# Kernel optimization log

Hardware: AMD Instinct MI355X
Metric: run time of the kernel (lower is better)

The kernel has to match this reference:

```python
import jax, jax.numpy as jnp
import numpy as np

B, H, W, D, HEADS, WS, SHIFT = 64, 28, 28, 384, 12, 7, 3
N = WS * WS  # tokens per window = 49
HEAD_DIM = D // HEADS
SCALE = HEAD_DIM ** -0.5


def _rel_pos_index():
    # standard Swin relative position index, shape [N, N], values in [0, (2*WS-1)^2)
    coords = np.stack(np.meshgrid(np.arange(WS), np.arange(WS), indexing='ij'))  # [2,ws,ws]
    cf = coords.reshape(2, -1)  # [2, N]
    rel = (cf[:, :, None] - cf[:, None, :]).transpose(1, 2, 0).astype(np.int64)  # [N,N,2]
    rel[:, :, 0] += WS - 1
    rel[:, :, 1] += WS - 1
    rel[:, :, 0] *= 2 * WS - 1
    return rel.sum(-1)  # [N, N]


def _attn_mask():
    # shifted-window mask, shape [nW, N, N], entries 0 or -100
    img = np.zeros((H, W))
    cnt = 0
    sl = (slice(0, -WS), slice(-WS, -SHIFT), slice(-SHIFT, None))
    for hs in sl:
        for ws_ in sl:
            img[hs, ws_] = cnt
            cnt += 1
    mw = img.reshape(H // WS, WS, W // WS, WS).transpose(0, 2, 1, 3).reshape(-1, N)  # [nW, N]
    diff = mw[:, None, :] - mw[:, :, None]  # unsqueeze(1) - unsqueeze(2)
    return np.where(diff != 0, -100.0, 0.0).astype(np.float32)


_REL_IDX = _rel_pos_index()
_ATTN_MASK = _attn_mask()


def _ln(x, g, b, eps=1e-5):
    m = x.mean(-1, keepdims=True)
    v = ((x - m) ** 2).mean(-1, keepdims=True)
    return (x - m) * jax.lax.rsqrt(v + eps) * g + b


def _window_partition(x):
    # [B,H,W,C] -> [B*nW, N, C]
    Bz, _, _, C = x.shape
    x = x.reshape(Bz, H // WS, WS, W // WS, WS, C).transpose(0, 1, 3, 2, 4, 5)
    return x.reshape(-1, N, C)


def _window_reverse(xw, Bz):
    # [B*nW, N, C] -> [B,H,W,C]
    C = xw.shape[-1]
    x = xw.reshape(Bz, H // WS, W // WS, WS, WS, C).transpose(0, 1, 3, 2, 4, 5)
    return x.reshape(Bz, H, W, C)


def setup_inputs() -> dict:
    key = jax.random.key(0)
    ks = jax.random.split(key, 12)
    s = 0.02
    return {
        'x': jax.random.normal(ks[0], (B, H * W, D), jnp.float32),
        'norm1_g': jnp.ones((D,), jnp.float32),
        'norm1_b': jnp.zeros((D,), jnp.float32),
        'qkv_w': jax.random.normal(ks[1], (D, 3 * D), jnp.float32) * s,
        'qkv_b': jnp.zeros((3 * D,), jnp.float32),
        'proj_w': jax.random.normal(ks[2], (D, D), jnp.float32) * s,
        'proj_b': jnp.zeros((D,), jnp.float32),
        'rpb_table': jax.random.normal(ks[3], ((2 * WS - 1) ** 2, HEADS), jnp.float32) * s,
        'norm2_g': jnp.ones((D,), jnp.float32),
        'norm2_b': jnp.zeros((D,), jnp.float32),
        'fc1_w': jax.random.normal(ks[4], (D, 4 * D), jnp.float32) * s,
        'fc1_b': jnp.zeros((4 * D,), jnp.float32),
        'fc2_w': jax.random.normal(ks[5], (4 * D, D), jnp.float32) * s,
        'fc2_b': jnp.zeros((D,), jnp.float32),
    }


def reference(x, norm1_g, norm1_b, qkv_w, qkv_b, proj_w, proj_b, rpb_table,
              norm2_g, norm2_b, fc1_w, fc1_b, fc2_w, fc2_b):
    Bz = x.shape[0]
    nW = (H // WS) * (W // WS)
    shortcut = x
    h = _ln(x, norm1_g, norm1_b).reshape(Bz, H, W, D)
    # cyclic shift
    h = jnp.roll(h, shift=(-SHIFT, -SHIFT), axis=(1, 2))
    xw = _window_partition(h)  # [B*nW, N, D]
    # windowed attention
    qkv = (xw @ qkv_w + qkv_b).reshape(-1, N, 3, HEADS, HEAD_DIM)
    q, k, v = [qkv[:, :, i].transpose(0, 2, 1, 3) for i in range(3)]  # [B*nW, H, N, hd]
    attn = jnp.einsum('whnd,whmd->whnm', q * SCALE, k)
    bias = rpb_table[jnp.asarray(_REL_IDX)]  # [N,N,HEADS]
    attn = attn + bias.transpose(2, 0, 1)[None]
    mask = jnp.asarray(_ATTN_MASK)  # [nW,N,N]
    attn = attn.reshape(Bz, nW, HEADS, N, N) + mask[None, :, None]
    attn = jax.nn.softmax(attn.reshape(-1, HEADS, N, N), axis=-1)
    out = jnp.einsum('whnm,whmd->whnd', attn, v)  # [B*nW, H, N, hd]
    out = out.transpose(0, 2, 1, 3).reshape(-1, N, D)
    out = out @ proj_w + proj_b
    # reverse windows + reverse shift
    h = _window_reverse(out, Bz)
    h = jnp.roll(h, shift=(SHIFT, SHIFT), axis=(1, 2)).reshape(Bz, H * W, D)
    x = shortcut + h
    # MLP
    m = _ln(x, norm2_g, norm2_b)
    m = jax.nn.gelu(m @ fc1_w + fc1_b, approximate=False)
    m = m @ fc2_w + fc2_b
    return x + m
```

## Files before the change

kernel.cpp:

```cpp
#include <hip/hip_runtime.h>

typedef unsigned short u16;
typedef unsigned int u32;
typedef __bf16 bf16x8 __attribute__((ext_vector_type(8)));
typedef float f32x4 __attribute__((ext_vector_type(4)));
typedef u32 u32x4 __attribute__((ext_vector_type(4)));
typedef u32 u32x2 __attribute__((ext_vector_type(2)));

union U8 { u32x4 u; u16 us[8]; bf16x8 bf; };

static __device__ __forceinline__ float b2f(u16 h) {
  union { u32 i; float f; } c; c.i = ((u32)h) << 16; return c.f;
}
static __device__ __forceinline__ u16 f2b(float f) {
  union { float f; u32 i; } c; c.f = f;
  u32 x = c.i;
  return (u16)((x + 0x7fffu + ((x >> 16) & 1u)) >> 16);
}
static __device__ __forceinline__ u32 pk2(float a, float b) {
  u32 d;
  asm("v_cvt_pk_bf16_f32 %0, %1, %2" : "=v"(d) : "v"(a), "v"(b));
  return d;
}
static __device__ __forceinline__ float gelu_f(float v) {
  float v2 = v * v;
  float ny2 = -2.0f * v * fmaf(0.0356774081f, v2, 0.7978845608f);
  float sig = __builtin_amdgcn_rcpf(1.0f + __expf(ny2));
  return v * sig;
}

#define G2LDS16(gp, lp)                                                                   \
  __builtin_amdgcn_global_load_lds((const __attribute__((address_space(1))) void*)(gp),   \
                                   (__attribute__((address_space(3))) void*)(lp), 16, 0, 0)

__global__ __launch_bounds__(256) void wtrans(const float* __restrict__ W, u16* __restrict__ WT,
                                              int K, int N) {
  __shared__ float t[32][33];
  int n0 = blockIdx.x * 32, k0 = blockIdx.y * 32;
  int tx = threadIdx.x, ty = threadIdx.y;
#pragma unroll
  for (int r = 0; r < 4; ++r)
    t[ty + 8 * r][tx] = W[(long)(k0 + ty + 8 * r) * N + n0 + tx];
  __syncthreads();
#pragma unroll
  for (int r = 0; r < 4; ++r)
    WT[(long)(n0 + ty + 8 * r) * K + k0 + tx] = f2b(t[tx][ty + 8 * r]);
}

template<int MODE>
__global__ __launch_bounds__(256) void ln_kernel(const float* __restrict__ src,
                                                 const float* __restrict__ g,
                                                 const float* __restrict__ b,
                                                 u16* __restrict__ dst) {
  int tok = blockIdx.x * 4 + (threadIdx.x >> 6);
  int lane = threadIdx.x & 63;
  long srow;
  if (MODE == 0) {
    int wg = tok / 49, i = tok % 49;
    int bimg = wg >> 4, wloc = wg & 15;
    int wh = wloc >> 2, ww = wloc & 3;
    int ih = i / 7, iw = i % 7;
    int hr = wh * 7 + ih + 3; if (hr >= 28) hr -= 28;
    int wr = ww * 7 + iw + 3; if (wr >= 28) wr -= 28;
    srow = (long)(bimg * 784 + hr * 28 + wr) * 384;
  } else {
    srow = (long)tok * 384;
  }
  const float* p = src + srow;
  float v[6];
#pragma unroll
  for (int t = 0; t < 3; ++t) {
    float2 z = *(const float2*)(p + (lane + 64 * t) * 2);
    v[2 * t] = z.x; v[2 * t + 1] = z.y;
  }
  float s = 0.f, ss = 0.f;
#pragma unroll
  for (int t = 0; t < 6; ++t) { s += v[t]; ss += v[t] * v[t]; }
  for (int m = 32; m; m >>= 1) { s += __shfl_xor(s, m); ss += __shfl_xor(ss, m); }
  float mean = s * (1.0f / 384.0f);
  float var  = ss * (1.0f / 384.0f) - mean * mean;
  float rs = rsqrtf(var + 1e-5f);
  u16* o = dst + (long)tok * 384;
#pragma unroll
  for (int t = 0; t < 3; ++t) {
    int ch = (lane + 64 * t) * 2;
    float2 gg = *(const float2*)(g + ch);
    float2 bb = *(const float2*)(b + ch);
    float r0 = (v[2 * t] - mean) * rs * gg.x + bb.x;
    float r1 = (v[2 * t + 1] - mean) * rs * gg.y + bb.y;
    *(u32*)&o[ch] = pk2(r0, r1);
  }
}

template<int EPI>
__global__ __launch_bounds__(256, 2) void gemm_big(
    const u16* __restrict__ A, const u16* __restrict__ BT,
    const float* __restrict__ bias, const float* __restrict__ xres,
    u16* __restrict__ Cb, float* __restrict__ Cf, int N, int K) {
  __shared__ __align__(16) u16 As0[128 * 64];
  __shared__ __align__(16) u16 As1[128 * 64];
  __shared__ __align__(16) u16 Bs0[128 * 64];
  __shared__ __align__(16) u16 Bs1[128 * 64];
  const int tid = threadIdx.x;
  const int wave = tid >> 6, lane = tid & 63, quad = lane >> 4, col = lane & 15;

  const int NY = (EPI == 0) ? 9 : (EPI == 1) ? 12 : 3;
  const int nwg = gridDim.x * gridDim.y;
  const int id = blockIdx.x + blockIdx.y * gridDim.x;
  const int sid = (id & 7) * (nwg >> 3) + (id >> 3);
  const int mi = sid / NY, ni = sid - mi * NY;
  const long m0 = (long)mi * 128;
  const int n0 = ni * 128;

  const int rm = (wave & 1) * 64, cn = (wave >> 1) * 64;
  f32x4 acc[4][4];
#pragma unroll
  for (int j = 0; j < 4; ++j)
#pragma unroll
    for (int i = 0; i < 4; ++i) acc[j][i] = f32x4{0.f, 0.f, 0.f, 0.f};

  const int K64 = K >> 6;
  const int sr = lane >> 3;
  const int sc = (lane & 7) ^ sr;
  const u16* gA = A  + (m0 + wave * 32 + sr) * (long)K + sc * 8;
  const u16* gB = BT + ((long)(n0 + wave * 32 + sr)) * K + sc * 8;

#define STAGE(kt, AS, BS)                                                        \
  {                                                                              \
    _Pragma("unroll")                                                            \
    for (int c = 0; c < 4; ++c) {                                                \
      G2LDS16(gA + (long)c * 8 * K + (kt) * 64, &AS[wave * 2048 + c * 512]);     \
      G2LDS16(gB + (long)c * 8 * K + (kt) * 64, &BS[wave * 2048 + c * 512]);     \
    }                                                                            \
  }

#define COMPUTE(AS, BS)                                                          \
  {                                                                              \
    _Pragma("unroll")                                                            \
    for (int kk = 0; kk < 2; ++kk) {                                             \
      U8 af[4], bfr[4];                                                          \
      _Pragma("unroll")                                                          \
      for (int i = 0; i < 4; ++i) {                                              \
        int row = rm + i * 16 + col;                                             \
        int slot = (kk * 4 + quad) ^ (row & 7);                                  \
        af[i].u = *(const u32x4*)&AS[row * 64 + slot * 8];                       \
      }                                                                          \
      _Pragma("unroll")                                                          \
      for (int j = 0; j < 4; ++j) {                                              \
        int row = cn + j * 16 + col;                                             \
        int slot = (kk * 4 + quad) ^ (row & 7);                                  \
        bfr[j].u = *(const u32x4*)&BS[row * 64 + slot * 8];                      \
      }                                                                          \
      _Pragma("unroll")                                                          \
      for (int j = 0; j < 4; ++j)                                                \
        _Pragma("unroll")                                                        \
        for (int i = 0; i < 4; ++i)                                              \
          acc[j][i] = __builtin_amdgcn_mfma_f32_16x16x32_bf16(bfr[j].bf, af[i].bf, acc[j][i], 0, 0, 0); \
    }                                                                            \
  }

  STAGE(0, As0, Bs0);
  __syncthreads();
  for (int kt = 0; kt < K64; kt += 2) {
    if (kt + 1 < K64) STAGE(kt + 1, As1, Bs1);
    COMPUTE(As0, Bs0);
    __syncthreads();
    if (kt + 2 < K64) STAGE(kt + 2, As0, Bs0);
    COMPUTE(As1, Bs1);
    __syncthreads();
  }
#undef STAGE
#undef COMPUTE

  if (EPI == 0 || EPI == 1) {
#pragma unroll
    for (int j = 0; j < 4; ++j) {
      int nb = n0 + cn + j * 16 + quad * 4;
      f32x4 bv = *(const f32x4*)&bias[nb];
#pragma unroll
      for (int i = 0; i < 4; ++i) {
        long row = m0 + rm + i * 16 + col;
        f32x4 v = acc[j][i] + bv;
        if (EPI == 1) {
#pragma unroll
          for (int r = 0; r < 4; ++r) v[r] = gelu_f(v[r]);
        }
        *(u32x2*)&Cb[row * N + nb] = u32x2{pk2(v[0], v[1]), pk2(v[2], v[3])};
      }
    }
  } else if (EPI == 2) {
#pragma unroll
    for (int i = 0; i < 4; ++i) {
      int row = (int)m0 + rm + i * 16 + col;
      int wg = row / 49, i49 = row - wg * 49;
      int bimg = wg >> 4, wloc = wg & 15;
      int wh = wloc >> 2, ww = wloc & 3;
      int ih = i49 / 7, iw = i49 - (i49 / 7) * 7;
      int ho = wh * 7 + ih + 3; if (ho >= 28) ho -= 28;
      int wo = ww * 7 + iw + 3; if (wo >= 28) wo -= 28;
      long dstb = (long)(bimg * 784 + ho * 28 + wo) * 384;
#pragma unroll
      for (int j = 0; j < 4; ++j) {
        int nb = n0 + cn + j * 16 + quad * 4;
        f32x4 bv = *(const f32x4*)&bias[nb];
        f32x4 xr = *(const f32x4*)&xres[dstb + nb];
        f32x4 v = acc[j][i] + bv + xr;
        *(f32x4*)&Cf[dstb + nb] = v;
      }
    }
  } else {
#pragma unroll
    for (int i = 0; i < 4; ++i) {
      long rb = (long)((int)m0 + rm + i * 16 + col) * 384;
#pragma unroll
      for (int j = 0; j < 4; ++j) {
        int nb = n0 + cn + j * 16 + quad * 4;
        f32x4 bv = *(const f32x4*)&bias[nb];
        f32x4 old = *(const f32x4*)&Cf[rb + nb];
        f32x4 v = acc[j][i] + bv + old;
        *(f32x4*)&Cf[rb + nb] = v;
      }
    }
  }
}

__global__ __launch_bounds__(256) void bmt_kernel(const float* __restrict__ rpb,
                                                  float* __restrict__ bmt) {
  int th = blockIdx.y;
  int type = th / 12, head = th - type * 12;
  int e = blockIdx.x * 256 + threadIdx.x;
  int tj = e >> 8, ti = (e >> 6) & 3, quad = (e >> 4) & 3, c = e & 15;
  int i = ti * 16 + c;
  int ih = i / 7, iw = i - ih * 7;
  int regi = ((type & 2) ? ((ih < 4) ? 1 : 2) : 0) * 3 + ((type & 1) ? ((iw < 4) ? 1 : 2) : 0);
  f32x4 v;
#pragma unroll
  for (int r = 0; r < 4; ++r) {
    int j = tj * 16 + quad * 4 + r;
    float val = -1e30f;
    if (i < 49 && j < 49) {
      int jh = j / 7, jw = j - jh * 7;
      int idx = (ih - jh + 6) * 13 + (iw - jw + 6);
      val = rpb[idx * 12 + head];
      int regj = ((type & 2) ? ((jh < 4) ? 1 : 2) : 0) * 3 + ((type & 1) ? ((jw < 4) ? 1 : 2) : 0);
      if (regi != regj) val -= 100.0f;
    }
    v[r] = val;
  }
  ((f32x4*)bmt)[((long)th * 16 + tj * 4 + ti) * 64 + quad * 16 + c] = v;
}

__global__ __launch_bounds__(256) void attn_kernel(const u16* __restrict__ qkv,
                                                   const float* __restrict__ bmt,
                                                   u16* __restrict__ obuf) {
  __shared__ __align__(16) u16 Ks[64 * 136];
  __shared__ __align__(16) u16 Vs[64 * 130];
  __shared__ __align__(16) u16 PL[4 * 64 * 72];
  const int w = blockIdx.x, h0 = blockIdx.y * 4;
  const int tid = threadIdx.x;
  const int hl = tid >> 6, lane = tid & 63, quad = lane >> 4, c = lane & 15;
  const int head = h0 + hl;
  const int wloc = w & 15;
  const int type = (((wloc >> 2) == 3) ? 2 : 0) + (((wloc & 3) == 3) ? 1 : 0);

#pragma unroll
  for (int it = 0; it < 4; ++it) {
    int cc = tid + it * 256;
    int j = cc >> 4, ch = cc & 15;
    u32x4 val = {0u, 0u, 0u, 0u};
    if (j < 49)
      val = *(const u32x4*)(qkv + ((long)w * 49 + j) * 1152 + 384 + h0 * 32 + ch * 8);
    *(u32x4*)&Ks[j * 136 + ch * 8] = val;
  }
#pragma unroll
  for (int it = 0; it < 16; ++it) {
    int cc = tid + it * 256;
    int j = cc >> 6, c4 = cc & 63;
    u32 val = 0u;
    if (j < 49)
      val = *(const u32*)(qkv + ((long)w * 49 + j) * 1152 + 768 + h0 * 32 + c4 * 2);
    *(u32*)&Vs[j * 130 + c4 * 2] = val;
  }

  U8 qf[4];
#pragma unroll
  for (int ti = 0; ti < 4; ++ti)
    qf[ti].u = *(const u32x4*)(qkv + ((long)w * 49 + ti * 16 + c) * 1152 + head * 32 + quad * 8);
  __syncthreads();

  U8 kf[4];
#pragma unroll
  for (int tj = 0; tj < 4; ++tj)
    kf[tj].u = *(const u32x4*)&Ks[(tj * 16 + c) * 136 + hl * 32 + quad * 8];
  f32x4 s[4][4];
#pragma unroll
  for (int tj = 0; tj < 4; ++tj)
#pragma unroll
    for (int ti = 0; ti < 4; ++ti)
      s[tj][ti] = __builtin_amdgcn_mfma_f32_16x16x32_bf16(kf[tj].bf, qf[ti].bf,
                                                          f32x4{0.f, 0.f, 0.f, 0.f}, 0, 0, 0);

  const f32x4* btb = (const f32x4*)bmt + ((long)(type * 12 + head) * 16) * 64 + quad * 16 + c;
#pragma unroll
  for (int tj = 0; tj < 4; ++tj)
#pragma unroll
    for (int ti = 0; ti < 4; ++ti) {
      f32x4 bv = btb[(tj * 4 + ti) * 64];
#pragma unroll
      for (int r = 0; r < 4; ++r)
        s[tj][ti][r] = fmaf(s[tj][ti][r], 0.17677669529663689f, bv[r]);
    }

#pragma unroll
  for (int ti = 0; ti < 4; ++ti) {
    float m = -1e30f;
#pragma unroll
    for (int tj = 0; tj < 4; ++tj)
#pragma unroll
      for (int r = 0; r < 4; ++r) m = fmaxf(m, s[tj][ti][r]);
    m = fmaxf(m, __shfl_xor(m, 16));
    m = fmaxf(m, __shfl_xor(m, 32));
    float l = 0.f;
#pragma unroll
    for (int tj = 0; tj < 4; ++tj)
#pragma unroll
      for (int r = 0; r < 4; ++r) {
        float p = __expf(s[tj][ti][r] - m);
        s[tj][ti][r] = p;
        l += p;
      }
    l += __shfl_xor(l, 16);
    l += __shfl_xor(l, 32);
    float inv = 1.0f / l;
#pragma unroll
    for (int tj = 0; tj < 4; ++tj)
#pragma unroll
      for (int r = 0; r < 4; ++r) s[tj][ti][r] *= inv;
  }

#pragma unroll
  for (int ti = 0; ti < 4; ++ti)
#pragma unroll
    for (int tj = 0; tj < 4; ++tj) {
      u32 lo = pk2(s[tj][ti][0], s[tj][ti][1]);
      u32 hi = pk2(s[tj][ti][2], s[tj][ti][3]);
      *(u32x2*)&PL[hl * 4608 + (ti * 16 + c) * 72 + tj * 16 + quad * 4] = u32x2{lo, hi};
    }

  f32x4 oacc[4][2];
#pragma unroll
  for (int t2 = 0; t2 < 4; ++t2) {
    oacc[t2][0] = f32x4{0.f, 0.f, 0.f, 0.f};
    oacc[t2][1] = f32x4{0.f, 0.f, 0.f, 0.f};
  }
#pragma unroll
  for (int kk = 0; kk < 2; ++kk) {
    U8 pa[4];
#pragma unroll
    for (int t2 = 0; t2 < 4; ++t2)
      pa[t2].u = *(const u32x4*)&PL[hl * 4608 + (t2 * 16 + c) * 72 + kk * 32 + quad * 8];
    U8 vf[2];
#pragma unroll
    for (int td = 0; td < 2; ++td)
#pragma unroll
      for (int e = 0; e < 8; ++e)
        vf[td].us[e] = Vs[(kk * 32 + quad * 8 + e) * 130 + hl * 32 + td * 16 + c];
#pragma unroll
    for (int t2 = 0; t2 < 4; ++t2)
#pragma unroll
      for (int td = 0; td < 2; ++td)
        oacc[t2][td] = __builtin_amdgcn_mfma_f32_16x16x32_bf16(pa[t2].bf, vf[td].bf, oacc[t2][td], 0, 0, 0);
  }

#pragma unroll
  for (int t2 = 0; t2 < 4; ++t2)
#pragma unroll
    for (int r = 0; r < 4; ++r) {
      int i = t2 * 16 + quad * 4 + r;
      if (i < 49) {
        u16* op = obuf + ((long)w * 49 + i) * 384 + head * 32 + c;
        op[0]  = f2b(oacc[t2][0][r]);
        op[16] = f2b(oacc[t2][1][r]);
      }
    }
}

extern "C" void kernel_launch(void* const* d_in, const int* in_sizes, int n_in,
                              void* d_out, int out_size, void* d_ws, size_t ws_size,
                              hipStream_t stream) {
  const float* x     = (const float*)d_in[0];
  const float* n1g   = (const float*)d_in[1];
  const float* n1b   = (const float*)d_in[2];
  const float* qkvw  = (const float*)d_in[3];
  const float* qkvb  = (const float*)d_in[4];
  const float* projw = (const float*)d_in[5];
  const float* projb = (const float*)d_in[6];
  const float* rpb   = (const float*)d_in[7];
  const float* n2g   = (const float*)d_in[8];
  const float* n2b   = (const float*)d_in[9];
  const float* fc1w  = (const float*)d_in[10];
  const float* fc1b  = (const float*)d_in[11];
  const float* fc2w  = (const float*)d_in[12];
  const float* fc2b  = (const float*)d_in[13];
  float* out = (float*)d_out;

  u16* qkvwT  = (u16*)d_ws;
  u16* projwT = qkvwT + 442368;
  u16* fc1wT  = projwT + 147456;
  u16* fc2wT  = fc1wT + 589824;
  u16* wsA    = fc2wT + 589824;
  u16* wsB    = wsA + 19267584;
  u16* xw   = wsA;
  u16* obuf = wsA;
  u16* abuf = wsA;
  u16* qkvB = wsB;
  u16* midB = wsB;
  float* bmtb = (float*)qkvwT;

  wtrans<<<dim3(36, 12), dim3(32, 8), 0, stream>>>(qkvw, qkvwT, 384, 1152);
  wtrans<<<dim3(12, 12), dim3(32, 8), 0, stream>>>(projw, projwT, 384, 384);
  wtrans<<<dim3(48, 12), dim3(32, 8), 0, stream>>>(fc1w, fc1wT, 384, 1536);
  wtrans<<<dim3(12, 48), dim3(32, 8), 0, stream>>>(fc2w, fc2wT, 1536, 384);

  ln_kernel<0><<<12544, 256, 0, stream>>>(x, n1g, n1b, xw);
  gemm_big<0><<<dim3(392, 9), 256, 0, stream>>>(xw, qkvwT, qkvb, nullptr, qkvB, nullptr, 1152, 384);
  bmt_kernel<<<dim3(4, 48), 256, 0, stream>>>(rpb, bmtb);
  attn_kernel<<<dim3(1024, 3), 256, 0, stream>>>(qkvB, bmtb, obuf);
  gemm_big<2><<<dim3(392, 3), 256, 0, stream>>>(obuf, projwT, projb, x, nullptr, out, 384, 384);
  ln_kernel<1><<<12544, 256, 0, stream>>>(out, n2g, n2b, abuf);
  gemm_big<1><<<dim3(392, 12), 256, 0, stream>>>(abuf, fc1wT, fc1b, nullptr, midB, nullptr, 1536, 384);
  gemm_big<3><<<dim3(392, 3), 256, 0, stream>>>(midB, fc2wT, fc2b, nullptr, nullptr, out, 384, 1536);
}
```

Before: 572.3 us.

## Single-buffer LDS in big GEMM to raise occupancy to four blocks per CU

```diff
diff --git a/kernel.cpp b/kernel.cpp
--- a/kernel.cpp
+++ b/kernel.cpp
@@ -93,14 +93,12 @@
 }
 
 template<int EPI>
-__global__ __launch_bounds__(256, 2) void gemm_big(
+__global__ __launch_bounds__(256, 4) void gemm_big(
     const u16* __restrict__ A, const u16* __restrict__ BT,
     const float* __restrict__ bias, const float* __restrict__ xres,
     u16* __restrict__ Cb, float* __restrict__ Cf, int N, int K) {
-  __shared__ __align__(16) u16 As0[128 * 64];
-  __shared__ __align__(16) u16 As1[128 * 64];
-  __shared__ __align__(16) u16 Bs0[128 * 64];
-  __shared__ __align__(16) u16 Bs1[128 * 64];
+  __shared__ __align__(16) u16 As[128 * 64];
+  __shared__ __align__(16) u16 Bs[128 * 64];
   const int tid = threadIdx.x;
   const int wave = tid >> 6, lane = tid & 63, quad = lane >> 4, col = lane & 15;
 
@@ -125,52 +123,36 @@
   const u16* gA = A  + (m0 + wave * 32 + sr) * (long)K + sc * 8;
   const u16* gB = BT + ((long)(n0 + wave * 32 + sr)) * K + sc * 8;
 
-#define STAGE(kt, AS, BS)                                                        \
-  {                                                                              \
-    _Pragma("unroll")                                                            \
-    for (int c = 0; c < 4; ++c) {                                                \
-      G2LDS16(gA + (long)c * 8 * K + (kt) * 64, &AS[wave * 2048 + c * 512]);     \
-      G2LDS16(gB + (long)c * 8 * K + (kt) * 64, &BS[wave * 2048 + c * 512]);     \
-    }                                                                            \
-  }
-
-#define COMPUTE(AS, BS)                                                          \
-  {                                                                              \
-    _Pragma("unroll")                                                            \
-    for (int kk = 0; kk < 2; ++kk) {                                             \
-      U8 af[4], bfr[4];                                                          \
-      _Pragma("unroll")                                                          \
-      for (int i = 0; i < 4; ++i) {                                              \
-        int row = rm + i * 16 + col;                                             \
-        int slot = (kk * 4 + quad) ^ (row & 7);                                  \
-        af[i].u = *(const u32x4*)&AS[row * 64 + slot * 8];                       \
-      }                                                                          \
-      _Pragma("unroll")                                                          \
-      for (int j = 0; j < 4; ++j) {                                              \
-        int row = cn + j * 16 + col;                                             \
-        int slot = (kk * 4 + quad) ^ (row & 7);                                  \
-        bfr[j].u = *(const u32x4*)&BS[row * 64 + slot * 8];                      \
-      }                                                                          \
-      _Pragma("unroll")                                                          \
-      for (int j = 0; j < 4; ++j)                                                \
-        _Pragma("unroll")                                                        \
-        for (int i = 0; i < 4; ++i)                                              \
-          acc[j][i] = __builtin_amdgcn_mfma_f32_16x16x32_bf16(bfr[j].bf, af[i].bf, acc[j][i], 0, 0, 0); \
-    }                                                                            \
-  }
-
-  STAGE(0, As0, Bs0);
-  __syncthreads();
-  for (int kt = 0; kt < K64; kt += 2) {
-    if (kt + 1 < K64) STAGE(kt + 1, As1, Bs1);
-    COMPUTE(As0, Bs0);
+  for (int kt = 0; kt < K64; ++kt) {
+    if (kt) __syncthreads();
+#pragma unroll
+    for (int c = 0; c < 4; ++c) {
+      G2LDS16(gA + (long)c * 8 * K + kt * 64, &As[wave * 2048 + c * 512]);
+      G2LDS16(gB + (long)c * 8 * K + kt * 64, &Bs[wave * 2048 + c * 512]);
+    }
     __syncthreads();
-    if (kt + 2 < K64) STAGE(kt + 2, As0, Bs0);
-    COMPUTE(As1, Bs1);
-    __syncthreads();
-  }
-#undef STAGE
-#undef COMPUTE
+#pragma unroll
+    for (int kk = 0; kk < 2; ++kk) {
+      U8 af[4], bfr[4];
+#pragma unroll
+      for (int i = 0; i < 4; ++i) {
+        int row = rm + i * 16 + col;
+        int slot = (kk * 4 + quad) ^ (row & 7);
+        af[i].u = *(const u32x4*)&As[row * 64 + slot * 8];
+      }
+#pragma unroll
+      for (int j = 0; j < 4; ++j) {
+        int row = cn + j * 16 + col;
+        int slot = (kk * 4 + quad) ^ (row & 7);
+        bfr[j].u = *(const u32x4*)&Bs[row * 64 + slot * 8];
+      }
+#pragma unroll
+      for (int j = 0; j < 4; ++j)
+#pragma unroll
+        for (int i = 0; i < 4; ++i)
+          acc[j][i] = __builtin_amdgcn_mfma_f32_16x16x32_bf16(bfr[j].bf, af[i].bf, acc[j][i], 0, 0, 0);
+    }
+  }
 
   if (EPI == 0 || EPI == 1) {
 #pragma unroll
```

After: 549.3 us. 1.04x faster.

## Deepen GEMM prefetch with manual vmcnt waits and fix XCD block remap

Applied to the files above, without the earlier changes.

```diff
diff --git a/kernel.cpp b/kernel.cpp
--- a/kernel.cpp
+++ b/kernel.cpp
@@ -98,16 +98,18 @@
     const float* __restrict__ bias, const float* __restrict__ xres,
     u16* __restrict__ Cb, float* __restrict__ Cf, int N, int K) {
   __shared__ __align__(16) u16 As0[128 * 64];
+  __shared__ __align__(16) u16 Bs0[128 * 64];
   __shared__ __align__(16) u16 As1[128 * 64];
-  __shared__ __align__(16) u16 Bs0[128 * 64];
   __shared__ __align__(16) u16 Bs1[128 * 64];
   const int tid = threadIdx.x;
   const int wave = tid >> 6, lane = tid & 63, quad = lane >> 4, col = lane & 15;
 
   const int NY = (EPI == 0) ? 9 : (EPI == 1) ? 12 : 3;
   const int nwg = gridDim.x * gridDim.y;
-  const int id = blockIdx.x + blockIdx.y * gridDim.x;
-  const int sid = (id & 7) * (nwg >> 3) + (id >> 3);
+  const int orig = blockIdx.x + blockIdx.y * gridDim.x;
+  const int q8 = nwg >> 3, r8 = nwg & 7;
+  const int xcd = orig & 7, idx = orig >> 3;
+  const int sid = (xcd < r8 ? xcd * (q8 + 1) : r8 * (q8 + 1) + (xcd - r8) * q8) + idx;
   const int mi = sid / NY, ni = sid - mi * NY;
   const long m0 = (long)mi * 128;
   const int n0 = ni * 128;
@@ -160,14 +162,28 @@
   }
 
   STAGE(0, As0, Bs0);
-  __syncthreads();
-  for (int kt = 0; kt < K64; kt += 2) {
-    if (kt + 1 < K64) STAGE(kt + 1, As1, Bs1);
+  STAGE(1, As1, Bs1);
+  for (int kt = 0; kt + 2 <= K64; kt += 2) {
+    asm volatile("s_waitcnt vmcnt(8)" ::: "memory");
+    __builtin_amdgcn_s_barrier();
+    __builtin_amdgcn_sched_barrier(0);
     COMPUTE(As0, Bs0);
-    __syncthreads();
-    if (kt + 2 < K64) STAGE(kt + 2, As0, Bs0);
+    __builtin_amdgcn_sched_barrier(0);
+    __builtin_amdgcn_s_barrier();
+    __builtin_amdgcn_sched_barrier(0);
+    if (kt + 2 < K64) {
+      STAGE(kt + 2, As0, Bs0);
+      asm volatile("s_waitcnt vmcnt(8)" ::: "memory");
+    } else {
+      asm volatile("s_waitcnt vmcnt(0)" ::: "memory");
+    }
+    __builtin_amdgcn_s_barrier();
+    __builtin_amdgcn_sched_barrier(0);
     COMPUTE(As1, Bs1);
-    __syncthreads();
+    __builtin_amdgcn_sched_barrier(0);
+    __builtin_amdgcn_s_barrier();
+    __builtin_amdgcn_sched_barrier(0);
+    if (kt + 3 < K64) STAGE(kt + 3, As1, Bs1);
   }
 #undef STAGE
 #undef COMPUTE
```

New measurement: 563.3 us. No clear change (-1.6%).
